# Kernel tuning notes

Measured on AMD Instinct MI355X. Metric: run time of the kernel, lower is better.

## Reference

```python
import jax, jax.numpy as jnp
import numpy as np


def setup_inputs() -> dict:
    key = jax.random.key(0)
    ks = jax.random.split(key, 6)
    C, C8, W, H, B = 512, 64, 64, 64, 4
    x = jax.random.normal(ks[0], (B, C, W, H), dtype=jnp.float32)
    Wf = jax.random.normal(ks[1], (C8, C), dtype=jnp.float32) * (1.0 / np.sqrt(C))
    Wg = jax.random.normal(ks[2], (C8, C), dtype=jnp.float32) * (1.0 / np.sqrt(C))
    Wh = jax.random.normal(ks[3], (C8, C), dtype=jnp.float32) * (1.0 / np.sqrt(C))
    Wv = jax.random.normal(ks[4], (C, C8), dtype=jnp.float32) * (1.0 / np.sqrt(C8))
    gamma = jax.random.normal(ks[5], (1,), dtype=jnp.float32)
    return {"x": x, "Wf": Wf, "Wg": Wg, "Wh": Wh, "Wv": Wv, "gamma": gamma}


def reference(x, Wf, Wg, Wh, Wv, gamma):
    b, c, w, h = x.shape
    n = w * h
    xf = x.reshape(b, c, n)                       # [b, c, n]
    # 1x1 convs == channel-mixing GEMMs
    f = jnp.einsum('oc,bcn->bon', Wf, xf)         # [b, c8, n]
    g = jnp.einsum('oc,bcn->bon', Wg, xf)         # [b, c8, n]
    hmap = jnp.einsum('oc,bcn->bon', Wh, xf)      # [b, c8, n]
    # attn_map[b, i, j] = sum_c f[b, c, i] * g[b, c, j]  (f permuted as in torch)
    attn = jnp.einsum('bci,bcj->bij', f, g)       # [b, n, n]
    # unconventional softmax over dim=1 (rows / the i axis)
    attn = jax.nn.softmax(attn, axis=1)
    sa = jnp.einsum('bcn,bnj->bcj', hmap, attn)   # [b, c8, n]
    sa = sa.reshape(b, -1, w, h)                  # [b, c8, w, h]
    sa = jnp.einsum('oc,bcwh->bowh', Wv, sa)      # [b, c, w, h]
    out = sa * gamma[0] + x
    return out, sa
```

## Files before the change

### kernel.cpp

```cpp
#include <hip/hip_runtime.h>
#include <cstddef>

#define BB 4
#define CC 512
#define NN 4096

using half8  = __attribute__((ext_vector_type(8))) _Float16;
using fp16x2 = __attribute__((ext_vector_type(2))) __fp16;
using short8 = __attribute__((ext_vector_type(8))) short;
using us8    = __attribute__((ext_vector_type(8))) unsigned short;
using f32x4  = __attribute__((ext_vector_type(4))) float;

__device__ __forceinline__ unsigned short f2bf(float x) {
    unsigned int u = __float_as_uint(x);
    u += 0x7fffu + ((u >> 16) & 1u);
    return (unsigned short)(u >> 16);
}

__global__ __launch_bounds__(256) void prep_kernel(
    const float* __restrict__ Wf, const float* __restrict__ Wg,
    const float* __restrict__ Wh, const float* __restrict__ Wv,
    _Float16* __restrict__ Wc16, _Float16* __restrict__ Wv16)
{
    int idx = blockIdx.x * 256 + threadIdx.x;
    int stride = gridDim.x * 256;
    const int N1 = 192 * 512, N2 = 512 * 64;
    for (int i = idx; i < N1 + N2; i += stride) {
        if (i < N1) {
            int row = i >> 9, c = i & 511;
            const float* src = (row < 64) ? Wf : ((row < 128) ? Wg : Wh);
            float sc = (row >= 64 && row < 128) ? 1.4426950408889634f : 1.0f;
            Wc16[i] = (_Float16)(sc * src[(row & 63) * 512 + c]);
        } else {
            int k = i - N1;
            Wv16[k] = (_Float16)Wv[k];
        }
    }
}

__global__ __launch_bounds__(256) void proj_kernel(
    const float* __restrict__ x, const _Float16* __restrict__ Wc16,
    _Float16* __restrict__ Kf, _Float16* __restrict__ Qf,
    unsigned short* __restrict__ Vt)
{
    __shared__ float xsT[2][16][68];
    const int t    = threadIdx.x;
    const int w    = t >> 6;
    const int lane = t & 63;
    const int lh   = lane & 15;
    const int qd   = lane >> 4;
    const int b    = blockIdx.x >> 8;
    const int i0   = (blockIdx.x & 255) << 4;

    f32x4 acc[3];
    #pragma unroll
    for (int ot = 0; ot < 3; ot++) { acc[ot][0]=0.f; acc[ot][1]=0.f; acc[ot][2]=0.f; acc[ot][3]=0.f; }

    const int ti = t & 3;
    const int tc = t >> 2;
    const float* xbase = x + (size_t)b*CC*NN + i0 + ti*4;

    float4 st = *(const float4*)(xbase + (size_t)tc*NN);
    xsT[0][ti*4+0][tc] = st.x; xsT[0][ti*4+1][tc] = st.y;
    xsT[0][ti*4+2][tc] = st.z; xsT[0][ti*4+3][tc] = st.w;
    __syncthreads();

    for (int ck = 0; ck < 8; ck++) {
        const int p = ck & 1;
        if (ck < 7) st = *(const float4*)(xbase + (size_t)((ck+1)*64 + tc)*NN);

        #pragma unroll
        for (int ks = 0; ks < 2; ks++) {
            half8 wf[3];
            #pragma unroll
            for (int ot = 0; ot < 3; ot++)
                wf[ot] = *(const half8*)(Wc16 + (size_t)(w*48 + ot*16 + lh)*512 + ck*64 + ks*32 + qd*8);
            const float* xr = &xsT[p][lh][ks*32 + qd*8];
            f32x4 xa = *(const f32x4*)xr;
            f32x4 xb = *(const f32x4*)(xr + 4);
            union { fp16x2 h2[4]; half8 h8; } u;
            u.h2[0] = __builtin_amdgcn_cvt_pkrtz(xa[0], xa[1]);
            u.h2[1] = __builtin_amdgcn_cvt_pkrtz(xa[2], xa[3]);
            u.h2[2] = __builtin_amdgcn_cvt_pkrtz(xb[0], xb[1]);
            u.h2[3] = __builtin_amdgcn_cvt_pkrtz(xb[2], xb[3]);
            #pragma unroll
            for (int ot = 0; ot < 3; ot++)
                acc[ot] = __builtin_amdgcn_mfma_f32_16x16x32_f16(wf[ot], u.h8, acc[ot], 0, 0, 0);
        }

        if (ck < 7) {
            const int q = p ^ 1;
            xsT[q][ti*4+0][tc] = st.x; xsT[q][ti*4+1][tc] = st.y;
            xsT[q][ti*4+2][tc] = st.z; xsT[q][ti*4+3][tc] = st.w;
        }
        __syncthreads();
    }

    #pragma unroll
    for (int ot = 0; ot < 3; ot++) {
        int g16 = w*3 + ot;
        int m   = g16 >> 2;
        int obase = (g16 & 3)*16 + qd*4;
        int ig = i0 + lh;
        #pragma unroll
        for (int r = 0; r < 4; r++) {
            float v = acc[ot][r];
            int ol = obase + r;
            if (m == 0)       Kf[((size_t)b*NN + ig)*64 + ol] = (_Float16)v;
            else if (m == 1)  Qf[((size_t)b*NN + ig)*64 + ol] = (_Float16)v;
            else              Vt[((size_t)b*64 + ol)*NN + ig] = f2bf(v);
        }
    }
}

__global__ __launch_bounds__(256) void attn_kernel(
    const _Float16* __restrict__ Kf, const _Float16* __restrict__ Qf,
    const unsigned short* __restrict__ Vt,
    _Float16* __restrict__ Po16, float* __restrict__ Pl)
{
    __shared__ __align__(16) unsigned short Kbuf[128*64];
    __shared__ __align__(16) unsigned short Vbuf[64*128];
    __shared__ __align__(16) unsigned short Psh[4][16*64];

    const int t    = threadIdx.x;
    const int wv   = t >> 6;
    const int lane = t & 63;
    const int lh   = lane & 15;
    const int qd   = lane >> 4;

    const int B   = blockIdx.x;
    const int xcd = B & 7;
    const int rr  = B >> 3;
    const int b   = xcd >> 1;
    const int jt  = (rr & 31)*2 + (xcd & 1);
    const int s   = rr >> 5;
    const int j0  = (jt << 6) + wv*16;

    const unsigned short* Kfu = (const unsigned short*)Kf;

    half8 qf0, qf1;
    {
        const size_t qb = ((size_t)b*NN + j0 + lh)*64 + qd*8;
        qf0 = *(const half8*)(Qf + qb);
        qf1 = *(const half8*)(Qf + qb + 32);
    }

    f32x4 o_acc[4];
    float l_r[4];
    #pragma unroll
    for (int dt = 0; dt < 4; dt++) { o_acc[dt][0]=0.f; o_acc[dt][1]=0.f; o_acc[dt][2]=0.f; o_acc[dt][3]=0.f; }
    #pragma unroll
    for (int r = 0; r < 4; r++) l_r[r] = 0.f;

    const int koff = s*1024;
    const int ki = t >> 3, kc = t & 7;
    const int vd = t >> 4, vc = t & 15;

#define LOADC(ck) do {                                                        \
    size_t kg = ((size_t)b*NN + koff + (ck)*128)*64;                          \
    size_t vg = (size_t)b*64*NN + koff + (ck)*128;                            \
    _Pragma("unroll")                                                         \
    for (int r_ = 0; r_ < 4; r_++) {                                          \
        kst[r_] = *(const us8*)(Kfu + kg + (size_t)(r_*32 + ki)*64 + kc*8);   \
        vst[r_] = *(const us8*)(Vt  + vg + (size_t)(r_*16 + vd)*NN + vc*8);   \
    } } while (0)

#define STOREC() do {                                                         \
    _Pragma("unroll")                                                         \
    for (int r_ = 0; r_ < 4; r_++) {                                          \
        int i_ = r_*32 + ki;                                                  \
        int d_ = r_*16 + vd;                                                  \
        *(us8*)(&Kbuf[i_*64  + ((kc ^ (i_ & 7))*8)])  = kst[r_];              \
        *(us8*)(&Vbuf[d_*128 + ((vc ^ (d_ & 15))*8)]) = vst[r_];              \
    } } while (0)

    us8 kst[4], vst[4];
    LOADC(0);
    STOREC();
    __syncthreads();

    for (int ck = 0; ck < 8; ck++) {
        if (ck < 7) LOADC(ck + 1);

        #pragma unroll
        for (int half = 0; half < 2; half++) {
            const unsigned short* Kb = &Kbuf[half*64*64];
            const unsigned short* Vb = &Vbuf[0];

            f32x4 sc[4];
            #pragma unroll
            for (int it = 0; it < 4; it++) {
                sc[it][0]=0.f; sc[it][1]=0.f; sc[it][2]=0.f; sc[it][3]=0.f;
                const unsigned short* kr = Kb + (it*16 + lh)*64;
                half8 k0 = *(const half8*)(kr + ((qd     ^ (lh & 7))*8));
                half8 k1 = *(const half8*)(kr + (((4+qd) ^ (lh & 7))*8));
                sc[it] = __builtin_amdgcn_mfma_f32_16x16x32_f16(qf0, k0, sc[it], 0,0,0);
                sc[it] = __builtin_amdgcn_mfma_f32_16x16x32_f16(qf1, k1, sc[it], 0,0,0);
            }

            #pragma unroll
            for (int it = 0; it < 4; it++)
                #pragma unroll
                for (int r = 0; r < 4; r++) {
                    float p_ = exp2f(sc[it][r]);
                    l_r[r] += p_;
                    int i_ = it*16 + lh;
                    int j_ = qd*4 + r;
                    Psh[wv][j_*64 + (((i_>>3) ^ (j_ & 7))*8) + (i_ & 7)] = f2bf(p_);
                }
            asm volatile("s_waitcnt lgkmcnt(0)" ::: "memory");

            short8 pf0 = *(const short8*)&Psh[wv][lh*64 + ((qd     ^ (lh & 7))*8)];
            short8 pf1 = *(const short8*)&Psh[wv][lh*64 + (((4+qd) ^ (lh & 7))*8)];

            #pragma unroll
            for (int dt = 0; dt < 4; dt++) {
                const unsigned short* vr = Vb + (dt*16 + lh)*128;
                short8 v0 = *(const short8*)(vr + (((half*8 + qd    ) ^ lh)*8));
                short8 v1 = *(const short8*)(vr + (((half*8 + 4 + qd) ^ lh)*8));
                o_acc[dt] = __builtin_amdgcn_mfma_f32_16x16x32_bf16(pf0, v0, o_acc[dt], 0,0,0);
                o_acc[dt] = __builtin_amdgcn_mfma_f32_16x16x32_bf16(pf1, v1, o_acc[dt], 0,0,0);
            }
        }

        __syncthreads();
        if (ck < 7) STOREC();
        __syncthreads();
    }
#undef LOADC
#undef STOREC

    float inv[4];
    #pragma unroll
    for (int r = 0; r < 4; r++) {
        float l = l_r[r];
        #pragma unroll
        for (int off = 1; off < 16; off <<= 1)
            l += __shfl_xor(l, off);
        l_r[r] = l;
        inv[r] = 1.0f / l;
    }
    const size_t pbase = ((size_t)(s*4 + b)*NN + j0);
    #pragma unroll
    for (int dt = 0; dt < 4; dt++)
        #pragma unroll
        for (int r = 0; r < 4; r++)
            Po16[(pbase + qd*4 + r)*64 + dt*16 + lh] = (_Float16)(o_acc[dt][r] * inv[r]);
    if (lh == 0) {
        #pragma unroll
        for (int r = 0; r < 4; r++)
            Pl[pbase + qd*4 + r] = l_r[r];
    }
}

__global__ __launch_bounds__(256) void outproj_kernel(
    const _Float16* __restrict__ Po16, const float* __restrict__ Pl,
    const _Float16* __restrict__ Wv16,
    const float* __restrict__ x, const float* __restrict__ gamma,
    float* __restrict__ out1, float* __restrict__ out2)
{
    const int t    = threadIdx.x;
    const int w    = t >> 6;
    const int lane = t & 63;
    const int lh   = lane & 15;
    const int qd   = lane >> 4;
    const int b    = blockIdx.x >> 7;
    const int j0   = (blockIdx.x & 127) << 5;
    const float g  = gamma[0];

    half8 sb[2][2];
    #pragma unroll
    for (int jt2 = 0; jt2 < 2; jt2++) {
        const int j = j0 + jt2*16 + lh;
        float os[16];
        #pragma unroll
        for (int k = 0; k < 16; k++) os[k] = 0.f;
        float lsum = 0.f;
        #pragma unroll
        for (int s = 0; s < 4; s++) {
            size_t base = ((size_t)(s*4 + b)*NN + j);
            half8 v0 = *(const half8*)(Po16 + base*64 + qd*8);
            half8 v1 = *(const half8*)(Po16 + base*64 + qd*8 + 32);
            float l = Pl[base];
            #pragma unroll
            for (int k = 0; k < 8; k++) {
                os[k]   = fmaf(l, (float)v0[k], os[k]);
                os[8+k] = fmaf(l, (float)v1[k], os[8+k]);
            }
            lsum += l;
        }
        float inv = 1.0f / lsum;
        union { fp16x2 h2[4]; half8 h8; } u0, u1;
        #pragma unroll
        for (int k = 0; k < 4; k++) {
            u0.h2[k] = __builtin_amdgcn_cvt_pkrtz(os[2*k]*inv,   os[2*k+1]*inv);
            u1.h2[k] = __builtin_amdgcn_cvt_pkrtz(os[8+2*k]*inv, os[8+2*k+1]*inv);
        }
        sb[jt2][0] = u0.h8;
        sb[jt2][1] = u1.h8;
    }

    #pragma unroll 2
    for (int ot8 = 0; ot8 < 8; ot8++) {
        const int ot = w*8 + ot8;
        const size_t wbase = (size_t)(ot*16 + lh)*64 + qd*8;
        half8 a0 = *(const half8*)(Wv16 + wbase);
        half8 a1 = *(const half8*)(Wv16 + wbase + 32);
        #pragma unroll
        for (int jt2 = 0; jt2 < 2; jt2++) {
            f32x4 acc; acc[0]=0.f; acc[1]=0.f; acc[2]=0.f; acc[3]=0.f;
            acc = __builtin_amdgcn_mfma_f32_16x16x32_f16(a0, sb[jt2][0], acc, 0, 0, 0);
            acc = __builtin_amdgcn_mfma_f32_16x16x32_f16(a1, sb[jt2][1], acc, 0, 0, 0);
            const int jg = j0 + jt2*16 + lh;
            #pragma unroll
            for (int r = 0; r < 4; r++) {
                const int o = ot*16 + qd*4 + r;
                size_t idx = ((size_t)b*CC + o)*NN + jg;
                float v = acc[r];
                out2[idx] = v;
                out1[idx] = fmaf(g, v, x[idx]);
            }
        }
    }
}

extern "C" void kernel_launch(void* const* d_in, const int* in_sizes, int n_in,
                              void* d_out, int out_size, void* d_ws, size_t ws_size,
                              hipStream_t stream) {
    const float* x     = (const float*)d_in[0];
    const float* Wf    = (const float*)d_in[1];
    const float* Wg    = (const float*)d_in[2];
    const float* Wh    = (const float*)d_in[3];
    const float* Wv    = (const float*)d_in[4];
    const float* gamma = (const float*)d_in[5];

    float* out1 = (float*)d_out;
    float* out2 = out1 + (size_t)BB*CC*NN;

    const size_t BND = (size_t)BB*NN*64;
    char* wp = (char*)d_ws;
    _Float16*       Kf   = (_Float16*)wp;        wp += BND*2;
    _Float16*       Qf   = (_Float16*)wp;        wp += BND*2;
    unsigned short* Vt   = (unsigned short*)wp;  wp += BND*2;
    _Float16*       Po16 = (_Float16*)wp;        wp += BND*4*2;
    float*          Pl   = (float*)wp;           wp += (size_t)4*BB*NN*4;
    _Float16*       Wc16 = (_Float16*)wp;        wp += (size_t)192*512*2;
    _Float16*       Wv16 = (_Float16*)wp;

    prep_kernel<<<dim3(64), dim3(256), 0, stream>>>(Wf, Wg, Wh, Wv, Wc16, Wv16);
    proj_kernel<<<dim3(BB*256), dim3(256), 0, stream>>>(x, Wc16, Kf, Qf, Vt);
    attn_kernel<<<dim3(BB*256), dim3(256), 0, stream>>>(Kf, Qf, Vt, Po16, Pl);
    outproj_kernel<<<dim3(512), dim3(256), 0, stream>>>(Po16, Pl, Wv16, x, gamma, out1, out2);
}
```

Before: 187.8 us.

## Widen proj tile with prefetched weights and coalesce outproj stores via LDS

The projection kernel now handles 32 positions per block instead of 16, so each weight fragment feeds two MFMAs. Weight fragments for the next channel chunk are register-prefetched alongside the x tile, which halves the grid and cuts redundant weight traffic. The output projection stages MFMA results in a per-wave LDS tile and then does float4 coalesced reads of x and writes of out1/out2, replacing scattered scalar stores. In exchange it uses more registers and LDS, and relies on s_waitcnt instead of barriers for intra-wave LDS ordering.

```diff
diff --git a/kernel.cpp b/kernel.cpp
--- a/kernel.cpp
+++ b/kernel.cpp
@@ -43,72 +43,108 @@
     _Float16* __restrict__ Kf, _Float16* __restrict__ Qf,
     unsigned short* __restrict__ Vt)
 {
-    __shared__ float xsT[2][16][68];
+    __shared__ float xsT[2][32][68];
     const int t    = threadIdx.x;
     const int w    = t >> 6;
     const int lane = t & 63;
     const int lh   = lane & 15;
     const int qd   = lane >> 4;
-    const int b    = blockIdx.x >> 8;
-    const int i0   = (blockIdx.x & 255) << 4;
-
-    f32x4 acc[3];
-    #pragma unroll
-    for (int ot = 0; ot < 3; ot++) { acc[ot][0]=0.f; acc[ot][1]=0.f; acc[ot][2]=0.f; acc[ot][3]=0.f; }
-
-    const int ti = t & 3;
-    const int tc = t >> 2;
-    const float* xbase = x + (size_t)b*CC*NN + i0 + ti*4;
-
-    float4 st = *(const float4*)(xbase + (size_t)tc*NN);
-    xsT[0][ti*4+0][tc] = st.x; xsT[0][ti*4+1][tc] = st.y;
-    xsT[0][ti*4+2][tc] = st.z; xsT[0][ti*4+3][tc] = st.w;
+    const int b    = blockIdx.x >> 7;
+    const int i0   = (blockIdx.x & 127) << 5;
+
+    f32x4 acc[3][2];
+    #pragma unroll
+    for (int ot = 0; ot < 3; ot++)
+        #pragma unroll
+        for (int it = 0; it < 2; it++) { acc[ot][it][0]=0.f; acc[ot][it][1]=0.f; acc[ot][it][2]=0.f; acc[ot][it][3]=0.f; }
+
+    const int ti8 = t & 7;
+    const int tc2 = t >> 3;
+    const float* xbase = x + (size_t)b*CC*NN + i0 + ti8*4;
+    const _Float16* wbase = Wc16 + (size_t)(w*48 + lh)*512 + qd*8;
+
+    float4 st0, st1;
+    half8  wcur[2][3], wnxt[2][3];
+
+#define LOADX(ck) do {                                                        \
+    st0 = *(const float4*)(xbase + (size_t)((ck)*64 + tc2)*NN);               \
+    st1 = *(const float4*)(xbase + (size_t)((ck)*64 + 32 + tc2)*NN);          \
+} while (0)
+#define STOREX(p_) do {                                                       \
+    xsT[p_][ti8*4+0][tc2]    = st0.x; xsT[p_][ti8*4+1][tc2]    = st0.y;       \
+    xsT[p_][ti8*4+2][tc2]    = st0.z; xsT[p_][ti8*4+3][tc2]    = st0.w;       \
+    xsT[p_][ti8*4+0][32+tc2] = st1.x; xsT[p_][ti8*4+1][32+tc2] = st1.y;       \
+    xsT[p_][ti8*4+2][32+tc2] = st1.z; xsT[p_][ti8*4+3][32+tc2] = st1.w;       \
+} while (0)
+#define LOADW(ck, WD) do {                                                    \
+    _Pragma("unroll")                                                         \
+    for (int ks_ = 0; ks_ < 2; ks_++)                                         \
+        _Pragma("unroll")                                                     \
+        for (int ot_ = 0; ot_ < 3; ot_++)                                     \
+            WD[ks_][ot_] = *(const half8*)(wbase + (size_t)(ot_*16)*512 + (ck)*64 + ks_*32); \
+} while (0)
+
+    LOADX(0); STOREX(0);
+    LOADW(0, wcur);
     __syncthreads();
 
+    #pragma unroll
     for (int ck = 0; ck < 8; ck++) {
         const int p = ck & 1;
-        if (ck < 7) st = *(const float4*)(xbase + (size_t)((ck+1)*64 + tc)*NN);
+        if (ck < 7) { LOADX(ck + 1); LOADW(ck + 1, wnxt); }
 
         #pragma unroll
         for (int ks = 0; ks < 2; ks++) {
-            half8 wf[3];
+            half8 xf[2];
+            #pragma unroll
+            for (int it = 0; it < 2; it++) {
+                const float* xr = &xsT[p][it*16 + lh][ks*32 + qd*8];
+                f32x4 xa = *(const f32x4*)xr;
+                f32x4 xb = *(const f32x4*)(xr + 4);
+                union { fp16x2 h2[4]; half8 h8; } u;
+                u.h2[0] = __builtin_amdgcn_cvt_pkrtz(xa[0], xa[1]);
+                u.h2[1] = __builtin_amdgcn_cvt_pkrtz(xa[2], xa[3]);
+                u.h2[2] = __builtin_amdgcn_cvt_pkrtz(xb[0], xb[1]);
+                u.h2[3] = __builtin_amdgcn_cvt_pkrtz(xb[2], xb[3]);
+                xf[it] = u.h8;
+            }
             #pragma unroll
             for (int ot = 0; ot < 3; ot++)
-                wf[ot] = *(const half8*)(Wc16 + (size_t)(w*48 + ot*16 + lh)*512 + ck*64 + ks*32 + qd*8);
-            const float* xr = &xsT[p][lh][ks*32 + qd*8];
-            f32x4 xa = *(const f32x4*)xr;
-            f32x4 xb = *(const f32x4*)(xr + 4);
-            union { fp16x2 h2[4]; half8 h8; } u;
-            u.h2[0] = __builtin_amdgcn_cvt_pkrtz(xa[0], xa[1]);
-            u.h2[1] = __builtin_amdgcn_cvt_pkrtz(xa[2], xa[3]);
-            u.h2[2] = __builtin_amdgcn_cvt_pkrtz(xb[0], xb[1]);
-            u.h2[3] = __builtin_amdgcn_cvt_pkrtz(xb[2], xb[3]);
-            #pragma unroll
-            for (int ot = 0; ot < 3; ot++)
-                acc[ot] = __builtin_amdgcn_mfma_f32_16x16x32_f16(wf[ot], u.h8, acc[ot], 0, 0, 0);
+                #pragma unroll
+                for (int it = 0; it < 2; it++)
+                    acc[ot][it] = __builtin_amdgcn_mfma_f32_16x16x32_f16(wcur[ks][ot], xf[it], acc[ot][it], 0, 0, 0);
         }
 
         if (ck < 7) {
-            const int q = p ^ 1;
-            xsT[q][ti*4+0][tc] = st.x; xsT[q][ti*4+1][tc] = st.y;
-            xsT[q][ti*4+2][tc] = st.z; xsT[q][ti*4+3][tc] = st.w;
+            STOREX(p ^ 1);
+            #pragma unroll
+            for (int ks_ = 0; ks_ < 2; ks_++)
+                #pragma unroll
+                for (int ot_ = 0; ot_ < 3; ot_++)
+                    wcur[ks_][ot_] = wnxt[ks_][ot_];
         }
         __syncthreads();
     }
+#undef LOADX
+#undef STOREX
+#undef LOADW
 
     #pragma unroll
     for (int ot = 0; ot < 3; ot++) {
         int g16 = w*3 + ot;
         int m   = g16 >> 2;
         int obase = (g16 & 3)*16 + qd*4;
-        int ig = i0 + lh;
-        #pragma unroll
-        for (int r = 0; r < 4; r++) {
-            float v = acc[ot][r];
-            int ol = obase + r;
-            if (m == 0)       Kf[((size_t)b*NN + ig)*64 + ol] = (_Float16)v;
-            else if (m == 1)  Qf[((size_t)b*NN + ig)*64 + ol] = (_Float16)v;
-            else              Vt[((size_t)b*64 + ol)*NN + ig] = f2bf(v);
+        #pragma unroll
+        for (int it = 0; it < 2; it++) {
+            int ig = i0 + it*16 + lh;
+            #pragma unroll
+            for (int r = 0; r < 4; r++) {
+                float v = acc[ot][it][r];
+                int ol = obase + r;
+                if (m == 0)       Kf[((size_t)b*NN + ig)*64 + ol] = (_Float16)v;
+                else if (m == 1)  Qf[((size_t)b*NN + ig)*64 + ol] = (_Float16)v;
+                else              Vt[((size_t)b*64 + ol)*NN + ig] = f2bf(v);
+            }
         }
     }
 }
@@ -259,6 +295,7 @@
     const float* __restrict__ x, const float* __restrict__ gamma,
     float* __restrict__ out1, float* __restrict__ out2)
 {
+    __shared__ float Osh[4][16][36];
     const int t    = threadIdx.x;
     const int w    = t >> 6;
     const int lane = t & 63;
@@ -300,27 +337,45 @@
         sb[jt2][1] = u1.h8;
     }
 
+    const int o_loc8 = lane >> 3;
+    const int j4     = (lane & 7) * 4;
+
     #pragma unroll 2
     for (int ot8 = 0; ot8 < 8; ot8++) {
         const int ot = w*8 + ot8;
         const size_t wbase = (size_t)(ot*16 + lh)*64 + qd*8;
         half8 a0 = *(const half8*)(Wv16 + wbase);
         half8 a1 = *(const half8*)(Wv16 + wbase + 32);
+
+        f32x4 acc[2];
         #pragma unroll
         for (int jt2 = 0; jt2 < 2; jt2++) {
-            f32x4 acc; acc[0]=0.f; acc[1]=0.f; acc[2]=0.f; acc[3]=0.f;
-            acc = __builtin_amdgcn_mfma_f32_16x16x32_f16(a0, sb[jt2][0], acc, 0, 0, 0);
-            acc = __builtin_amdgcn_mfma_f32_16x16x32_f16(a1, sb[jt2][1], acc, 0, 0, 0);
-            const int jg = j0 + jt2*16 + lh;
-            #pragma unroll
-            for (int r = 0; r < 4; r++) {
-                const int o = ot*16 + qd*4 + r;
-                size_t idx = ((size_t)b*CC + o)*NN + jg;
-                float v = acc[r];
-                out2[idx] = v;
-                out1[idx] = fmaf(g, v, x[idx]);
-            }
-        }
+            acc[jt2][0]=0.f; acc[jt2][1]=0.f; acc[jt2][2]=0.f; acc[jt2][3]=0.f;
+            acc[jt2] = __builtin_amdgcn_mfma_f32_16x16x32_f16(a0, sb[jt2][0], acc[jt2], 0, 0, 0);
+            acc[jt2] = __builtin_amdgcn_mfma_f32_16x16x32_f16(a1, sb[jt2][1], acc[jt2], 0, 0, 0);
+        }
+
+        #pragma unroll
+        for (int jt2 = 0; jt2 < 2; jt2++)
+            #pragma unroll
+            for (int r = 0; r < 4; r++)
+                Osh[w][qd*4 + r][jt2*16 + lh] = acc[jt2][r];
+        asm volatile("s_waitcnt lgkmcnt(0)" ::: "memory");
+
+        #pragma unroll
+        for (int rr2 = 0; rr2 < 2; rr2++) {
+            const int o_loc = o_loc8 + 8*rr2;
+            f32x4 v = *(const f32x4*)&Osh[w][o_loc][j4];
+            const int o  = ot*16 + o_loc;
+            const size_t idx = ((size_t)b*CC + o)*NN + j0 + j4;
+            f32x4 xv = *(const f32x4*)(x + idx);
+            *(f32x4*)(out2 + idx) = v;
+            f32x4 r1;
+            r1[0] = fmaf(g, v[0], xv[0]); r1[1] = fmaf(g, v[1], xv[1]);
+            r1[2] = fmaf(g, v[2], xv[2]); r1[3] = fmaf(g, v[3], xv[3]);
+            *(f32x4*)(out1 + idx) = r1;
+        }
+        asm volatile("s_waitcnt lgkmcnt(0)" ::: "memory");
     }
 }
 
@@ -348,7 +403,7 @@
     _Float16*       Wv16 = (_Float16*)wp;
 
     prep_kernel<<<dim3(64), dim3(256), 0, stream>>>(Wf, Wg, Wh, Wv, Wc16, Wv16);
-    proj_kernel<<<dim3(BB*256), dim3(256), 0, stream>>>(x, Wc16, Kf, Qf, Vt);
+    proj_kernel<<<dim3(BB*128), dim3(256), 0, stream>>>(x, Wc16, Kf, Qf, Vt);
     attn_kernel<<<dim3(BB*256), dim3(256), 0, stream>>>(Kf, Qf, Vt, Po16, Pl);
     outproj_kernel<<<dim3(512), dim3(256), 0, stream>>>(Po16, Pl, Wv16, x, gamma, out1, out2);
 }
```

After: 172.1 us. 1.09x faster.
